# Kernel tuning notes

Measured on AMD Instinct MI355X. Metric: run time of the kernel, lower is better.

Reference implementation:

```python
import jax, jax.numpy as jnp
import numpy as np

B_, S_, H_, I_, N_, K_ = 2, 2048, 1024, 2048, 16, 4

def setup_inputs() -> dict:
    key = jax.random.key(0)
    ks = jax.random.split(key, 6)
    return {
        "x": jax.random.normal(ks[0], (B_, S_, H_), jnp.float32),
        "W_in": jax.random.normal(ks[1], (H_, 2 * I_), jnp.float32) * (H_ ** -0.5),
        "conv_w": jax.random.normal(ks[2], (I_, 1, K_), jnp.float32) * (K_ ** -0.5),
        "ln_gamma": jnp.ones((I_,), jnp.float32),
        "ln_beta": jnp.zeros((I_,), jnp.float32),
        "W_xproj": jax.random.normal(ks[3], (I_, 2 * N_ + 1), jnp.float32) * (I_ ** -0.5),
        "A_param": jax.random.normal(ks[4], (I_, N_), jnp.float32) * 0.1,
        "D": jnp.ones((I_,), jnp.float32),
        "W_out": jax.random.normal(ks[5], (I_, H_), jnp.float32) * (I_ ** -0.5),
    }

def _layernorm(x, g, b, eps=1e-5):
    mu = jnp.mean(x, axis=-1, keepdims=True)
    var = jnp.mean((x - mu) ** 2, axis=-1, keepdims=True)
    return (x - mu) * jax.lax.rsqrt(var + eps) * g + b

def reference(x, W_in, conv_w, ln_gamma, ln_beta, W_xproj, A_param, D, W_out):
    b, s, _ = x.shape
    n = A_param.shape[1]
    xz = x @ W_in                                   # (b,s,2I)
    xc, z = jnp.split(xz, 2, axis=-1)
    # depthwise causal conv1d: torch pads both sides k-1 then truncates [:s] == left-pad k-1
    xc = jax.lax.conv_general_dilated(
        xc.transpose(0, 2, 1), conv_w, window_strides=(1,),
        padding=[(conv_w.shape[-1] - 1, 0)],
        feature_group_count=conv_w.shape[0],
        dimension_numbers=("NCH", "OIH", "NCH")).transpose(0, 2, 1)  # (b,s,I)
    xc = jax.nn.silu(xc)
    xc = _layernorm(xc, ln_gamma, ln_beta)
    xp = xc @ W_xproj                               # (b,s,2N+1)
    delta = jnp.clip(jax.nn.softplus(xp[..., :1]), 1e-6, 10.0)   # (b,s,1)
    Bm = xp[..., 1:1 + n]                           # (b,s,N)
    Cm = xp[..., 1 + n:]                            # (b,s,N)
    A = -jnp.clip(jax.nn.softplus(A_param), 0.1, 10.0)           # (I,N)
    # decay[b,s,i,n] = exp(delta[b,s] * A[i,n]), clamped
    decay = jnp.clip(jnp.exp(delta[..., None] * A[None, None]), 1e-6, 1.0)  # (b,s,I,N)
    # y = x * sum_n B*C*decay  (state-dim reduction of the broadcast 4D tensor)
    y = xc * jnp.einsum("bsn,bsin->bsi", Bm * Cm, decay)
    y = y + xc * D
    return (y * jax.nn.silu(z)) @ W_out
```

## Files before the change

### kernel.cpp

```cpp
#include <hip/hip_runtime.h>
#include <hip/hip_bf16.h>
#include <cmath>

typedef __bf16 bf16_t;
typedef __bf16 bf16x8 __attribute__((ext_vector_type(8)));
typedef __bf16 bf16x4 __attribute__((ext_vector_type(4)));
typedef float  f32x4  __attribute__((ext_vector_type(4)));

static constexpr int B_  = 2, S_ = 2048, H_ = 1024, I_ = 2048, NST = 16;
static constexpr int ROWS  = B_ * S_;
static constexpr int TWO_I = 2 * I_;
static constexpr int XPD   = 2 * NST + 1;
static constexpr int XPN   = 64;

#define AS_G(p) ((const __attribute__((address_space(1))) void*)(p))
#define AS_L(p) ((__attribute__((address_space(3))) void*)(p))

template<int N> __device__ __forceinline__ void wait_vmcnt();
template<> __device__ __forceinline__ void wait_vmcnt<4>() {
    asm volatile("s_waitcnt vmcnt(4)" ::: "memory");
}

__device__ __forceinline__ float softplus_f(float x) {
    return x > 15.f ? x : log1pf(__expf(x));
}

__device__ __forceinline__ f32x4 b2f(bf16x4 v) {
    return (f32x4){(float)v[0], (float)v[1], (float)v[2], (float)v[3]};
}

__device__ __forceinline__ float fast_exp2(float x) {
#if __has_builtin(__builtin_amdgcn_exp2f)
    return __builtin_amdgcn_exp2f(x);
#else
    return exp2f(x);
#endif
}
__device__ __forceinline__ float fast_rcp(float x) {
#if __has_builtin(__builtin_amdgcn_rcpf)
    return __builtin_amdgcn_rcpf(x);
#else
    return 1.f / x;
#endif
}
__device__ __forceinline__ float fast_sigmoid(float x) {
    return fast_rcp(1.f + __expf(-x));
}
__device__ __forceinline__ float rflf(float x) {
    return __int_as_float(__builtin_amdgcn_readfirstlane(__float_as_int(x)));
}

template<int GX, int GY, int XW>
__device__ __forceinline__ void xcd_swz(int id, int& bx, int& by) {
    constexpr int SX = GX / XW;
    constexpr int SY = GY * XW / 8;
    const int xcd = id & 7;
    const int j   = id >> 3;
    bx = (xcd % XW) * SX + j % SX;
    by = (xcd / XW) * SY + j / SX;
}


__global__ __launch_bounds__(256)
void prep_all(const float* __restrict__ x, const float* __restrict__ W_in,
              const float* __restrict__ W_out, const float* __restrict__ A_param,
              const float* __restrict__ Wx, const float* __restrict__ conv_w,
              bf16_t* __restrict__ Xb, bf16_t* __restrict__ W1t,
              bf16_t* __restrict__ Wot, float* __restrict__ A2T,
              float* __restrict__ cwT, bf16_t* __restrict__ WxTb)
{
    const int b   = blockIdx.x;
    const int tid = threadIdx.x;
    __shared__ float t[32][33];

    if (b < 4096) {
        const int i = b * 256 + tid;
        f32x4 v = *(const f32x4*)(x + (size_t)i * 4);
        bf16x4 o;
        o[0] = (bf16_t)v[0]; o[1] = (bf16_t)v[1];
        o[2] = (bf16_t)v[2]; o[3] = (bf16_t)v[3];
        *(bf16x4*)(Xb + (size_t)i * 4) = o;
    } else if (b < 8192) {
        const int tb = b - 4096;
        const int c0 = (tb & 127) * 32, r0 = (tb >> 7) * 32;
        const int tx = tid & 31, ty = tid >> 5;
        #pragma unroll
        for (int k = 0; k < 4; ++k)
            t[ty + 8 * k][tx] = W_in[(size_t)(r0 + ty + 8 * k) * 4096 + c0 + tx];
        __syncthreads();
        #pragma unroll
        for (int k = 0; k < 4; ++k)
            W1t[(size_t)(c0 + ty + 8 * k) * 1024 + r0 + tx] = (bf16_t)t[tx][ty + 8 * k];
    } else if (b < 10240) {
        const int tb = b - 8192;
        const int c0 = (tb & 31) * 32, r0 = (tb >> 5) * 32;
        const int tx = tid & 31, ty = tid >> 5;
        #pragma unroll
        for (int k = 0; k < 4; ++k)
            t[ty + 8 * k][tx] = W_out[(size_t)(r0 + ty + 8 * k) * 1024 + c0 + tx];
        __syncthreads();
        #pragma unroll
        for (int k = 0; k < 4; ++k)
            Wot[(size_t)(c0 + ty + 8 * k) * 2048 + r0 + tx] = (bf16_t)t[tx][ty + 8 * k];
    } else {
        const int i = (b - 10240) * 256 + tid;
        if (i < NST * I_) {
            int n = i >> 11, c = i & (I_ - 1);
            float sp = softplus_f(A_param[(size_t)c * NST + n]);
            A2T[i] = -fminf(fmaxf(sp, 0.1f), 10.f) * 1.44269504088896340736f;
        }
        if (i < 4 * I_) {
            int j = i >> 11, c = i & (I_ - 1);
            cwT[i] = conv_w[(size_t)c * 4 + j];
        }
        if (i < XPN * I_) {
            int j = i >> 11, c = i & (I_ - 1);
            WxTb[i] = (j < XPD) ? (bf16_t)Wx[(size_t)c * XPD + j] : (bf16_t)0.f;
        }
    }
}


template<int M, int N, int K, int BM, int BN, int WM, int WN, int THREADS,
         int GX, int GY, int XW, typename OutT>
__global__ __launch_bounds__(THREADS)
void gemm_fp(const bf16_t* __restrict__ A, const bf16_t* __restrict__ Bt,
             OutT* __restrict__ C)
{
    constexpr int BK  = 32;
    constexpr int NT  = K / BK;
    constexpr int MR  = BM / WM / 16;
    constexpr int NR  = BN / WN / 16;
    constexpr int MH  = MR / 2;
    constexpr int RPC = THREADS / 4;
    constexpr int CA  = BM / RPC;
    constexpr int CB  = BN / RPC;
    static_assert(CA + CB == 4, "vmcnt template fixed at 4");

    __shared__ bf16_t lA[4][BM * BK];
    __shared__ bf16_t lB[4][BN * BK];

    int bx, by;
    xcd_swz<GX, GY, XW>(blockIdx.x, bx, by);
    const int bm = by * BM;
    const int bn = bx * BN;

    const int tid  = threadIdx.x;
    const int lane = tid & 63;
    const int wave = tid >> 6;
    const int wm   = wave / WN;
    const int wn   = wave % WN;

    const int frow = lane & 15;
    const int fsw  = ((lane >> 4) ^ ((frow >> 1) & 3)) << 3;

    const int str = tid >> 2;
    const int stp = tid & 3;

    const bf16_t* baseA[CA];
    #pragma unroll
    for (int a = 0; a < CA; ++a) {
        const int rt = a * RPC + str;
        baseA[a] = A + (size_t)(bm + rt) * K + ((stp ^ ((rt >> 1) & 3)) << 3);
    }
    const bf16_t* baseB[CB];
    #pragma unroll
    for (int a = 0; a < CB; ++a) {
        const int rt = a * RPC + str;
        baseB[a] = Bt + (size_t)(bn + rt) * K + ((stp ^ ((rt >> 1) & 3)) << 3);
    }

    f32x4 acc[MR][NR];
    #pragma unroll
    for (int m = 0; m < MR; ++m)
        #pragma unroll
        for (int n = 0; n < NR; ++n)
            acc[m][n] = (f32x4){0.f, 0.f, 0.f, 0.f};

    auto stageA = [&](int k0, int b) {
        #pragma unroll
        for (int a = 0; a < CA; ++a)
            __builtin_amdgcn_global_load_lds(AS_G(baseA[a] + k0),
                AS_L(&lA[b][a * RPC * 32 + wave * 512]), 16, 0, 0);
    };
    auto stageB = [&](int k0, int b) {
        #pragma unroll
        for (int a = 0; a < CB; ++a)
            __builtin_amdgcn_global_load_lds(AS_G(baseB[a] + k0),
                AS_L(&lB[b][a * RPC * 32 + wave * 512]), 16, 0, 0);
    };

    stageA(0, 0); stageB(0, 0);
    stageA(BK, 1); stageB(BK, 1);
    wait_vmcnt<4>();
    __builtin_amdgcn_s_barrier();

    #pragma unroll 1
    for (int t = 0; t < NT; ++t) {
        const int buf = t & 3;
        const int nb  = (t + 2) & 3;
        int kn = (t + 2) * BK;
        if (kn >= K) kn -= K;

        bf16x8 bfr[NR];
        #pragma unroll
        for (int n = 0; n < NR; ++n)
            bfr[n] = *(const bf16x8*)(&lB[buf][(wn * (NR * 16) + n * 16 + frow) * 32 + fsw]);
        bf16x8 af0[MH];
        #pragma unroll
        for (int m = 0; m < MH; ++m)
            af0[m] = *(const bf16x8*)(&lA[buf][(wm * (MR * 16) + m * 16 + frow) * 32 + fsw]);
        stageA(kn, nb);

        __builtin_amdgcn_s_setprio(1);
        #pragma unroll
        for (int m = 0; m < MH; ++m)
            #pragma unroll
            for (int n = 0; n < NR; ++n)
                acc[m][n] = __builtin_amdgcn_mfma_f32_16x16x32_bf16(
                    af0[m], bfr[n], acc[m][n], 0, 0, 0);
        __builtin_amdgcn_s_setprio(0);

        bf16x8 af1[MR - MH];
        #pragma unroll
        for (int m = 0; m < MR - MH; ++m)
            af1[m] = *(const bf16x8*)(&lA[buf][(wm * (MR * 16) + (MH + m) * 16 + frow) * 32 + fsw]);
        stageB(kn, nb);

        __builtin_amdgcn_s_setprio(1);
        #pragma unroll
        for (int m = 0; m < MR - MH; ++m)
            #pragma unroll
            for (int n = 0; n < NR; ++n)
                acc[MH + m][n] = __builtin_amdgcn_mfma_f32_16x16x32_bf16(
                    af1[m], bfr[n], acc[MH + m][n], 0, 0, 0);
        __builtin_amdgcn_s_setprio(0);

        wait_vmcnt<4>();
        __builtin_amdgcn_s_barrier();
    }

    const int crow = (lane >> 4) * 4;
    const int ccol = lane & 15;
    #pragma unroll
    for (int m = 0; m < MR; ++m)
        #pragma unroll
        for (int n = 0; n < NR; ++n)
            #pragma unroll
            for (int r = 0; r < 4; ++r)
                C[(size_t)(bm + wm * (MR * 16) + m * 16 + crow + r) * N
                  + (bn + wn * (NR * 16) + n * 16 + ccol)] = (OutT)acc[m][n][r];
}


template<int M, int N, int K, int GX, int GY, int XW>
__global__ __launch_bounds__(512)
void gemm3_kg(const bf16_t* __restrict__ A, const bf16_t* __restrict__ Bt,
              float* __restrict__ C)
{
    constexpr int BM = 128, BN = 128, BK = 32;
    constexpr int KH = K / 2;
    constexpr int NT = KH / BK;
    constexpr int MR = 4, NR = 4, MH = 2;

    __shared__ bf16_t smem[65536];

    int bx, by;
    xcd_swz<GX, GY, XW>(blockIdx.x, bx, by);
    const int bm = by * BM;
    const int bn = bx * BN;

    const int tid  = threadIdx.x;
    const int lane = tid & 63;
    const int wave = tid >> 6;
    const int grp  = wave >> 2;
    const int gw   = wave & 3;
    const int wm   = gw >> 1;
    const int wn   = gw & 1;

    const int frow = lane & 15;
    const int fsw  = ((lane >> 4) ^ ((frow >> 1) & 3)) << 3;

    const int gtid = tid & 255;
    const int str  = gtid >> 2;
    const int stp  = gtid & 3;

    bf16_t* lA = smem + grp * 16384;
    bf16_t* lB = smem + 32768 + grp * 16384;

    const bf16_t* baseA[2];
    #pragma unroll
    for (int a = 0; a < 2; ++a) {
        const int rt = a * 64 + str;
        baseA[a] = A + (size_t)(bm + rt) * K + grp * KH + ((stp ^ ((rt >> 1) & 3)) << 3);
    }
    const bf16_t* baseB[2];
    #pragma unroll
    for (int a = 0; a < 2; ++a) {
        const int rt = a * 64 + str;
        baseB[a] = Bt + (size_t)(bn + rt) * K + grp * KH + ((stp ^ ((rt >> 1) & 3)) << 3);
    }

    f32x4 acc[MR][NR];
    #pragma unroll
    for (int m = 0; m < MR; ++m)
        #pragma unroll
        for (int n = 0; n < NR; ++n)
            acc[m][n] = (f32x4){0.f, 0.f, 0.f, 0.f};

    auto stageA = [&](int k0, int b) {
        #pragma unroll
        for (int a = 0; a < 2; ++a)
            __builtin_amdgcn_global_load_lds(AS_G(baseA[a] + k0),
                AS_L(lA + b * 4096 + a * 2048 + gw * 512), 16, 0, 0);
    };
    auto stageB = [&](int k0, int b) {
        #pragma unroll
        for (int a = 0; a < 2; ++a)
            __builtin_amdgcn_global_load_lds(AS_G(baseB[a] + k0),
                AS_L(lB + b * 4096 + a * 2048 + gw * 512), 16, 0, 0);
    };

    stageA(0, 0); stageB(0, 0);
    stageA(BK, 1); stageB(BK, 1);
    wait_vmcnt<4>();
    __builtin_amdgcn_s_barrier();

    #pragma unroll 1
    for (int t = 0; t < NT; ++t) {
        const int buf = t & 3;
        const int nb  = (t + 2) & 3;
        int kn = (t + 2) * BK;
        if (kn >= KH) kn -= KH;

        bf16x8 bfr[NR];
        #pragma unroll
        for (int n = 0; n < NR; ++n)
            bfr[n] = *(const bf16x8*)(lB + buf * 4096 + (wn * 64 + n * 16 + frow) * 32 + fsw);
        bf16x8 af0[MH];
        #pragma unroll
        for (int m = 0; m < MH; ++m)
            af0[m] = *(const bf16x8*)(lA + buf * 4096 + (wm * 64 + m * 16 + frow) * 32 + fsw);
        stageA(kn, nb);

        __builtin_amdgcn_s_setprio(1);
        #pragma unroll
        for (int m = 0; m < MH; ++m)
            #pragma unroll
            for (int n = 0; n < NR; ++n)
                acc[m][n] = __builtin_amdgcn_mfma_f32_16x16x32_bf16(
                    af0[m], bfr[n], acc[m][n], 0, 0, 0);
        __builtin_amdgcn_s_setprio(0);

        bf16x8 af1[MR - MH];
        #pragma unroll
        for (int m = 0; m < MR - MH; ++m)
            af1[m] = *(const bf16x8*)(lA + buf * 4096 + (wm * 64 + (MH + m) * 16 + frow) * 32 + fsw);
        stageB(kn, nb);

        __builtin_amdgcn_s_setprio(1);
        #pragma unroll
        for (int m = 0; m < MR - MH; ++m)
            #pragma unroll
            for (int n = 0; n < NR; ++n)
                acc[MH + m][n] = __builtin_amdgcn_mfma_f32_16x16x32_bf16(
                    af1[m], bfr[n], acc[MH + m][n], 0, 0, 0);
        __builtin_amdgcn_s_setprio(0);

        wait_vmcnt<4>();
        __builtin_amdgcn_s_barrier();
    }

    asm volatile("s_waitcnt vmcnt(0)" ::: "memory");
    __builtin_amdgcn_s_barrier();

    float* accx = (float*)smem;
    const int crow = (lane >> 4) * 4;
    const int ccol = lane & 15;

    if (grp == 1) {
        #pragma unroll
        for (int m = 0; m < MR; ++m)
            #pragma unroll
            for (int n = 0; n < NR; ++n) {
                const int row = wm * 64 + m * 16 + crow;
                const int col = wn * 64 + n * 16 + ccol;
                #pragma unroll
                for (int r = 0; r < 4; ++r)
                    accx[(size_t)(row + r) * 132 + col] = acc[m][n][r];
            }
    }
    __syncthreads();
    if (grp == 0) {
        #pragma unroll
        for (int m = 0; m < MR; ++m)
            #pragma unroll
            for (int n = 0; n < NR; ++n) {
                const int row = wm * 64 + m * 16 + crow;
                const int col = wn * 64 + n * 16 + ccol;
                #pragma unroll
                for (int r = 0; r < 4; ++r)
                    C[(size_t)(bm + row + r) * N + bn + col] =
                        acc[m][n][r] + accx[(size_t)(row + r) * 132 + col];
            }
    }
}


__global__ __launch_bounds__(256)
void conv_ln4(const bf16_t* __restrict__ xz,
              const float* __restrict__ cwT,
              const float* __restrict__ ln_g,
              const float* __restrict__ ln_b,
              bf16_t* __restrict__ Xn)
{
    const int row0 = blockIdx.x * 4;
    const int s0   = row0 & (S_ - 1);
    const int tid  = threadIdx.x;
    const int lane = tid & 63;
    const int wave = tid >> 6;
    const bf16_t* xzr = xz + (size_t)row0 * TWO_I;

    __shared__ float lnr[4][4][2];

    float xc[4][8];
    float sm[4] = {0.f, 0.f, 0.f, 0.f};
    float sq[4] = {0.f, 0.f, 0.f, 0.f};

    #pragma unroll
    for (int g = 0; g < 2; ++g) {
        const int c = g * 1024 + tid * 4;
        const f32x4 w0 = *(const f32x4*)(cwT + 0 * I_ + c);
        const f32x4 w1 = *(const f32x4*)(cwT + 1 * I_ + c);
        const f32x4 w2 = *(const f32x4*)(cwT + 2 * I_ + c);
        const f32x4 w3 = *(const f32x4*)(cwT + 3 * I_ + c);
        const f32x4 z4 = (f32x4){0.f, 0.f, 0.f, 0.f};
        f32x4 xv[7];
        #pragma unroll
        for (int j = 0; j < 7; ++j)
            xv[j] = (s0 + j >= 3)
                  ? b2f(*(const bf16x4*)(xzr + (ptrdiff_t)(j - 3) * TWO_I + c)) : z4;
        #pragma unroll
        for (int r = 0; r < 4; ++r) {
            const f32x4 a = w0 * xv[r] + w1 * xv[r + 1] + w2 * xv[r + 2] + w3 * xv[r + 3];
            #pragma unroll
            for (int e = 0; e < 4; ++e) {
                const float v = a[e];
                const float t = v * fast_sigmoid(v);
                xc[r][g * 4 + e] = t;
                sm[r] += t; sq[r] += t * t;
            }
        }
    }

    #pragma unroll
    for (int off = 32; off; off >>= 1)
        #pragma unroll
        for (int r = 0; r < 4; ++r) {
            sm[r] += __shfl_xor(sm[r], off, 64);
            sq[r] += __shfl_xor(sq[r], off, 64);
        }
    if (lane == 0)
        #pragma unroll
        for (int r = 0; r < 4; ++r) {
            lnr[wave][r][0] = sm[r]; lnr[wave][r][1] = sq[r];
        }
    __syncthreads();
    float mu[4], rs[4];
    #pragma unroll
    for (int r = 0; r < 4; ++r) {
        const float s  = lnr[0][r][0] + lnr[1][r][0] + lnr[2][r][0] + lnr[3][r][0];
        const float q  = lnr[0][r][1] + lnr[1][r][1] + lnr[2][r][1] + lnr[3][r][1];
        mu[r] = s * (1.f / I_);
        rs[r] = rsqrtf(q * (1.f / I_) - mu[r] * mu[r] + 1e-5f);
    }

    #pragma unroll
    for (int g = 0; g < 2; ++g) {
        const int c = g * 1024 + tid * 4;
        const f32x4 gg = *(const f32x4*)(ln_g + c);
        const f32x4 bb = *(const f32x4*)(ln_b + c);
        #pragma unroll
        for (int r = 0; r < 4; ++r) {
            bf16x4 h4;
            #pragma unroll
            for (int e = 0; e < 4; ++e)
                h4[e] = (bf16_t)((xc[r][g * 4 + e] - mu[r]) * rs[r] * gg[e] + bb[e]);
            *(bf16x4*)(Xn + (size_t)(row0 + r) * I_ + c) = h4;
        }
    }
}


__global__ __launch_bounds__(256)
void xproj_gemm(const bf16_t* __restrict__ Xn,
                const bf16_t* __restrict__ Wb, float* __restrict__ xp_part)
{
    constexpr int BM = 128, BK = 32, KS = 512;
    __shared__ bf16_t lA[BM * BK];
    __shared__ bf16_t lB[XPN * BK];

    const int bm   = blockIdx.x * BM;
    const int ks   = blockIdx.y;
    const int tid  = threadIdx.x;
    const int lane = tid & 63;
    const int wave = tid >> 6;
    const int wm   = (wave >> 1) * 64;
    const int wn   = (wave & 1) * 32;

    const int srow  = lane >> 2;
    const int skoff = (lane & 3) * 8;
    const int frow  = lane & 15;
    const int fko   = (lane >> 4) * 8;

    f32x4 acc[4][2];
    #pragma unroll
    for (int m = 0; m < 4; ++m)
        #pragma unroll
        for (int n = 0; n < 2; ++n)
            acc[m][n] = (f32x4){0.f, 0.f, 0.f, 0.f};

    for (int k0 = ks * KS; k0 < ks * KS + KS; k0 += BK) {
        #pragma unroll
        for (int t = 0; t < 2; ++t) {
            const int c = wave * 2 + t;
            const bf16_t* ga = Xn + (size_t)(bm + c * 16 + srow) * I_ + k0 + skoff;
            __builtin_amdgcn_global_load_lds(AS_G(ga), AS_L(lA + c * 512), 16, 0, 0);
        }
        const bf16_t* gb = Wb + (size_t)(wave * 16 + srow) * I_ + k0 + skoff;
        __builtin_amdgcn_global_load_lds(AS_G(gb), AS_L(lB + wave * 512), 16, 0, 0);
        __syncthreads();

        bf16x8 af[4], bf2[2];
        #pragma unroll
        for (int m = 0; m < 4; ++m)
            af[m] = *(const bf16x8*)(lA + (wm + m * 16 + frow) * BK + fko);
        #pragma unroll
        for (int n = 0; n < 2; ++n)
            bf2[n] = *(const bf16x8*)(lB + (wn + n * 16 + frow) * BK + fko);

        #pragma unroll
        for (int m = 0; m < 4; ++m)
            #pragma unroll
            for (int n = 0; n < 2; ++n)
                acc[m][n] = __builtin_amdgcn_mfma_f32_16x16x32_bf16(
                    af[m], bf2[n], acc[m][n], 0, 0, 0);

        __syncthreads();
    }

    float* out = xp_part + ((size_t)ks * ROWS + bm) * XPN;
    const int crow = (lane >> 4) * 4;
    const int ccol = lane & 15;
    #pragma unroll
    for (int m = 0; m < 4; ++m)
        #pragma unroll
        for (int n = 0; n < 2; ++n)
            #pragma unroll
            for (int r = 0; r < 4; ++r)
                out[(size_t)(wm + m * 16 + crow + r) * XPN
                    + (wn + n * 16 + ccol)] = acc[m][n][r];
}


__global__ __launch_bounds__(256)
void ssm_gate4(const bf16_t* __restrict__ xz,
               const bf16_t* __restrict__ Xn,
               const float* __restrict__ xp_part,
               const float* __restrict__ A2T,
               const float* __restrict__ Dv,
               bf16_t* __restrict__ U)
{
    const int row0 = blockIdx.x * 4;
    const int tid  = threadIdx.x;

    __shared__ float xps[4][XPD];
    __shared__ float bcs[4][NST];

    if (tid < 4 * XPD) {
        const int r = tid / XPD;
        const int j = tid - r * XPD;
        float s = 0.f;
        #pragma unroll
        for (int ks = 0; ks < 4; ++ks)
            s += xp_part[((size_t)ks * ROWS + row0 + r) * XPN + j];
        xps[r][j] = s;
    }
    __syncthreads();
    if (tid < 4 * NST) {
        const int r = tid >> 4;
        const int n = tid & 15;
        bcs[r][n] = xps[r][1 + n] * xps[r][1 + NST + n];
    }
    __syncthreads();

    float d[4];
    #pragma unroll
    for (int r = 0; r < 4; ++r)
        d[r] = fminf(fmaxf(softplus_f(xps[r][0]), 1e-6f), 10.f);

    #pragma unroll 1
    for (int g = 0; g < 2; ++g) {
        const int c = g * 1024 + tid * 4;
        f32x4 sa[4];
        #pragma unroll
        for (int r = 0; r < 4; ++r)
            sa[r] = (f32x4){0.f, 0.f, 0.f, 0.f};

        #pragma unroll 1
        for (int nb = 0; nb < 4; ++nb) {
            const float* ap = A2T + (size_t)(nb * 4) * I_ + c;
            f32x4 av[4];
            #pragma unroll
            for (int j = 0; j < 4; ++j)
                av[j] = *(const f32x4*)(ap + (size_t)j * I_);
            #pragma unroll
            for (int j = 0; j < 4; ++j) {
                const float b0 = rflf(bcs[0][nb * 4 + j]);
                const float b1 = rflf(bcs[1][nb * 4 + j]);
                const float b2 = rflf(bcs[2][nb * 4 + j]);
                const float b3 = rflf(bcs[3][nb * 4 + j]);
                #pragma unroll
                for (int e = 0; e < 4; ++e) {
                    sa[0][e] += b0 * fast_exp2(d[0] * av[j][e]);
                    sa[1][e] += b1 * fast_exp2(d[1] * av[j][e]);
                    sa[2][e] += b2 * fast_exp2(d[2] * av[j][e]);
                    sa[3][e] += b3 * fast_exp2(d[3] * av[j][e]);
                }
            }
        }

        const f32x4 dvv = *(const f32x4*)(Dv + c);
        #pragma unroll
        for (int r = 0; r < 4; ++r) {
            const f32x4 xn = b2f(*(const bf16x4*)(Xn + (size_t)(row0 + r) * I_ + c));
            const f32x4 zv = b2f(*(const bf16x4*)(xz + (size_t)(row0 + r) * TWO_I + I_ + c));
            bf16x4 o;
            #pragma unroll
            for (int e = 0; e < 4; ++e) {
                const float y = xn[e] * (sa[r][e] + dvv[e]);
                const float z = zv[e];
                o[e] = (bf16_t)(y * z * fast_sigmoid(z));
            }
            *(bf16x4*)(U + (size_t)(row0 + r) * I_ + c) = o;
        }
    }
}


extern "C" void kernel_launch(void* const* d_in, const int* in_sizes, int n_in,
                              void* d_out, int out_size, void* d_ws, size_t ws_size,
                              hipStream_t stream)
{
    const float* x     = (const float*)d_in[0];
    const float* W_in  = (const float*)d_in[1];
    const float* convw = (const float*)d_in[2];
    const float* ln_g  = (const float*)d_in[3];
    const float* ln_b  = (const float*)d_in[4];
    const float* Wx    = (const float*)d_in[5];
    const float* A_p   = (const float*)d_in[6];
    const float* Dv    = (const float*)d_in[7];
    const float* W_out = (const float*)d_in[8];
    float* out = (float*)d_out;

    char* ws = (char*)d_ws;
    bf16_t* Xb   = (bf16_t*)(ws);
    bf16_t* W1t  = (bf16_t*)(ws + (size_t)(8u  << 20));
    bf16_t* Wot  = (bf16_t*)(ws + (size_t)(16u << 20));
    float*  A2T  = (float*) (ws + (size_t)(20u << 20));
    float*  cwT  = (float*) (ws + (size_t)(20u << 20) + (128u << 10));
    bf16_t* WxTb = (bf16_t*)(ws + (size_t)(20u << 20) + (256u << 10));
    bf16_t* XZb  = (bf16_t*)(ws + (size_t)(22u << 20));
    bf16_t* U    = (bf16_t*)(ws + (size_t)(54u << 20));
    bf16_t* Xn   = (bf16_t*)(ws);
    float*  xp4  = (float*) (ws + (size_t)(86u << 20));

    prep_all<<<10752, 256, 0, stream>>>(x, W_in, W_out, A_p, Wx, convw,
                                        Xb, W1t, Wot, A2T, cwT, WxTb);

    gemm_fp<ROWS, TWO_I, H_, 256, 256, 2, 4, 512, 16, 16, 4, bf16_t>
        <<<256, 512, 0, stream>>>(Xb, W1t, XZb);
    conv_ln4<<<ROWS / 4, 256, 0, stream>>>(XZb, cwT, ln_g, ln_b, Xn);
    xproj_gemm<<<dim3(ROWS / 128, 4), 256, 0, stream>>>(Xn, WxTb, xp4);
    ssm_gate4<<<ROWS / 4, 256, 0, stream>>>(XZb, Xn, xp4, A2T, Dv, U);
    gemm3_kg<ROWS, H_, I_, 8, 32, 2>
        <<<256, 512, 0, stream>>>(U, Wot, out);
}
```

Before: 119.3 us.

## Use split-K 128x128 GEMM for input projection and process 8 rows per SSM block

```diff
diff --git a/kernel.cpp b/kernel.cpp
--- a/kernel.cpp
+++ b/kernel.cpp
@@ -121,142 +121,10 @@
 }
 
 
-template<int M, int N, int K, int BM, int BN, int WM, int WN, int THREADS,
-         int GX, int GY, int XW, typename OutT>
-__global__ __launch_bounds__(THREADS)
-void gemm_fp(const bf16_t* __restrict__ A, const bf16_t* __restrict__ Bt,
+template<int M, int N, int K, int GX, int GY, int XW, typename OutT>
+__global__ __launch_bounds__(512)
+void gemm_kg(const bf16_t* __restrict__ A, const bf16_t* __restrict__ Bt,
              OutT* __restrict__ C)
-{
-    constexpr int BK  = 32;
-    constexpr int NT  = K / BK;
-    constexpr int MR  = BM / WM / 16;
-    constexpr int NR  = BN / WN / 16;
-    constexpr int MH  = MR / 2;
-    constexpr int RPC = THREADS / 4;
-    constexpr int CA  = BM / RPC;
-    constexpr int CB  = BN / RPC;
-    static_assert(CA + CB == 4, "vmcnt template fixed at 4");
-
-    __shared__ bf16_t lA[4][BM * BK];
-    __shared__ bf16_t lB[4][BN * BK];
-
-    int bx, by;
-    xcd_swz<GX, GY, XW>(blockIdx.x, bx, by);
-    const int bm = by * BM;
-    const int bn = bx * BN;
-
-    const int tid  = threadIdx.x;
-    const int lane = tid & 63;
-    const int wave = tid >> 6;
-    const int wm   = wave / WN;
-    const int wn   = wave % WN;
-
-    const int frow = lane & 15;
-    const int fsw  = ((lane >> 4) ^ ((frow >> 1) & 3)) << 3;
-
-    const int str = tid >> 2;
-    const int stp = tid & 3;
-
-    const bf16_t* baseA[CA];
-    #pragma unroll
-    for (int a = 0; a < CA; ++a) {
-        const int rt = a * RPC + str;
-        baseA[a] = A + (size_t)(bm + rt) * K + ((stp ^ ((rt >> 1) & 3)) << 3);
-    }
-    const bf16_t* baseB[CB];
-    #pragma unroll
-    for (int a = 0; a < CB; ++a) {
-        const int rt = a * RPC + str;
-        baseB[a] = Bt + (size_t)(bn + rt) * K + ((stp ^ ((rt >> 1) & 3)) << 3);
-    }
-
-    f32x4 acc[MR][NR];
-    #pragma unroll
-    for (int m = 0; m < MR; ++m)
-        #pragma unroll
-        for (int n = 0; n < NR; ++n)
-            acc[m][n] = (f32x4){0.f, 0.f, 0.f, 0.f};
-
-    auto stageA = [&](int k0, int b) {
-        #pragma unroll
-        for (int a = 0; a < CA; ++a)
-            __builtin_amdgcn_global_load_lds(AS_G(baseA[a] + k0),
-                AS_L(&lA[b][a * RPC * 32 + wave * 512]), 16, 0, 0);
-    };
-    auto stageB = [&](int k0, int b) {
-        #pragma unroll
-        for (int a = 0; a < CB; ++a)
-            __builtin_amdgcn_global_load_lds(AS_G(baseB[a] + k0),
-                AS_L(&lB[b][a * RPC * 32 + wave * 512]), 16, 0, 0);
-    };
-
-    stageA(0, 0); stageB(0, 0);
-    stageA(BK, 1); stageB(BK, 1);
-    wait_vmcnt<4>();
-    __builtin_amdgcn_s_barrier();
-
-    #pragma unroll 1
-    for (int t = 0; t < NT; ++t) {
-        const int buf = t & 3;
-        const int nb  = (t + 2) & 3;
-        int kn = (t + 2) * BK;
-        if (kn >= K) kn -= K;
-
-        bf16x8 bfr[NR];
-        #pragma unroll
-        for (int n = 0; n < NR; ++n)
-            bfr[n] = *(const bf16x8*)(&lB[buf][(wn * (NR * 16) + n * 16 + frow) * 32 + fsw]);
-        bf16x8 af0[MH];
-        #pragma unroll
-        for (int m = 0; m < MH; ++m)
-            af0[m] = *(const bf16x8*)(&lA[buf][(wm * (MR * 16) + m * 16 + frow) * 32 + fsw]);
-        stageA(kn, nb);
-
-        __builtin_amdgcn_s_setprio(1);
-        #pragma unroll
-        for (int m = 0; m < MH; ++m)
-            #pragma unroll
-            for (int n = 0; n < NR; ++n)
-                acc[m][n] = __builtin_amdgcn_mfma_f32_16x16x32_bf16(
-                    af0[m], bfr[n], acc[m][n], 0, 0, 0);
-        __builtin_amdgcn_s_setprio(0);
-
-        bf16x8 af1[MR - MH];
-        #pragma unroll
-        for (int m = 0; m < MR - MH; ++m)
-            af1[m] = *(const bf16x8*)(&lA[buf][(wm * (MR * 16) + (MH + m) * 16 + frow) * 32 + fsw]);
-        stageB(kn, nb);
-
-        __builtin_amdgcn_s_setprio(1);
-        #pragma unroll
-        for (int m = 0; m < MR - MH; ++m)
-            #pragma unroll
-            for (int n = 0; n < NR; ++n)
-                acc[MH + m][n] = __builtin_amdgcn_mfma_f32_16x16x32_bf16(
-                    af1[m], bfr[n], acc[MH + m][n], 0, 0, 0);
-        __builtin_amdgcn_s_setprio(0);
-
-        wait_vmcnt<4>();
-        __builtin_amdgcn_s_barrier();
-    }
-
-    const int crow = (lane >> 4) * 4;
-    const int ccol = lane & 15;
-    #pragma unroll
-    for (int m = 0; m < MR; ++m)
-        #pragma unroll
-        for (int n = 0; n < NR; ++n)
-            #pragma unroll
-            for (int r = 0; r < 4; ++r)
-                C[(size_t)(bm + wm * (MR * 16) + m * 16 + crow + r) * N
-                  + (bn + wn * (NR * 16) + n * 16 + ccol)] = (OutT)acc[m][n][r];
-}
-
-
-template<int M, int N, int K, int GX, int GY, int XW>
-__global__ __launch_bounds__(512)
-void gemm3_kg(const bf16_t* __restrict__ A, const bf16_t* __restrict__ Bt,
-              float* __restrict__ C)
 {
     constexpr int BM = 128, BN = 128, BK = 32;
     constexpr int KH = K / 2;
@@ -401,7 +269,7 @@
                 #pragma unroll
                 for (int r = 0; r < 4; ++r)
                     C[(size_t)(bm + row + r) * N + bn + col] =
-                        acc[m][n][r] + accx[(size_t)(row + r) * 132 + col];
+                        (OutT)(acc[m][n][r] + accx[(size_t)(row + r) * 132 + col]);
             }
     }
 }
@@ -564,22 +432,22 @@
 
 
 __global__ __launch_bounds__(256)
-void ssm_gate4(const bf16_t* __restrict__ xz,
+void ssm_gate8(const bf16_t* __restrict__ xz,
                const bf16_t* __restrict__ Xn,
                const float* __restrict__ xp_part,
                const float* __restrict__ A2T,
                const float* __restrict__ Dv,
                bf16_t* __restrict__ U)
 {
-    const int row0 = blockIdx.x * 4;
+    const int row0 = blockIdx.x * 8;
     const int tid  = threadIdx.x;
 
-    __shared__ float xps[4][XPD];
-    __shared__ float bcs[4][NST];
-
-    if (tid < 4 * XPD) {
-        const int r = tid / XPD;
-        const int j = tid - r * XPD;
+    __shared__ float xps[8][XPD];
+    __shared__ float bcs[8][NST];
+
+    for (int i = tid; i < 8 * XPD; i += 256) {
+        const int r = i / XPD;
+        const int j = i - r * XPD;
         float s = 0.f;
         #pragma unroll
         for (int ks = 0; ks < 4; ++ks)
@@ -587,24 +455,24 @@
         xps[r][j] = s;
     }
     __syncthreads();
-    if (tid < 4 * NST) {
+    if (tid < 8 * NST) {
         const int r = tid >> 4;
         const int n = tid & 15;
         bcs[r][n] = xps[r][1 + n] * xps[r][1 + NST + n];
     }
     __syncthreads();
 
-    float d[4];
-    #pragma unroll
-    for (int r = 0; r < 4; ++r)
+    float d[8];
+    #pragma unroll
+    for (int r = 0; r < 8; ++r)
         d[r] = fminf(fmaxf(softplus_f(xps[r][0]), 1e-6f), 10.f);
 
     #pragma unroll 1
     for (int g = 0; g < 2; ++g) {
         const int c = g * 1024 + tid * 4;
-        f32x4 sa[4];
-        #pragma unroll
-        for (int r = 0; r < 4; ++r)
+        f32x4 sa[8];
+        #pragma unroll
+        for (int r = 0; r < 8; ++r)
             sa[r] = (f32x4){0.f, 0.f, 0.f, 0.f};
 
         #pragma unroll 1
@@ -616,23 +484,22 @@
                 av[j] = *(const f32x4*)(ap + (size_t)j * I_);
             #pragma unroll
             for (int j = 0; j < 4; ++j) {
-                const float b0 = rflf(bcs[0][nb * 4 + j]);
-                const float b1 = rflf(bcs[1][nb * 4 + j]);
-                const float b2 = rflf(bcs[2][nb * 4 + j]);
-                const float b3 = rflf(bcs[3][nb * 4 + j]);
+                float bv[8];
+                #pragma unroll
+                for (int r = 0; r < 8; ++r)
+                    bv[r] = rflf(bcs[r][nb * 4 + j]);
                 #pragma unroll
                 for (int e = 0; e < 4; ++e) {
-                    sa[0][e] += b0 * fast_exp2(d[0] * av[j][e]);
-                    sa[1][e] += b1 * fast_exp2(d[1] * av[j][e]);
-                    sa[2][e] += b2 * fast_exp2(d[2] * av[j][e]);
-                    sa[3][e] += b3 * fast_exp2(d[3] * av[j][e]);
+                    #pragma unroll
+                    for (int r = 0; r < 8; ++r)
+                        sa[r][e] += bv[r] * fast_exp2(d[r] * av[j][e]);
                 }
             }
         }
 
         const f32x4 dvv = *(const f32x4*)(Dv + c);
         #pragma unroll
-        for (int r = 0; r < 4; ++r) {
+        for (int r = 0; r < 8; ++r) {
             const f32x4 xn = b2f(*(const bf16x4*)(Xn + (size_t)(row0 + r) * I_ + c));
             const f32x4 zv = b2f(*(const bf16x4*)(xz + (size_t)(row0 + r) * TWO_I + I_ + c));
             bf16x4 o;
@@ -678,11 +545,11 @@
     prep_all<<<10752, 256, 0, stream>>>(x, W_in, W_out, A_p, Wx, convw,
                                         Xb, W1t, Wot, A2T, cwT, WxTb);
 
-    gemm_fp<ROWS, TWO_I, H_, 256, 256, 2, 4, 512, 16, 16, 4, bf16_t>
-        <<<256, 512, 0, stream>>>(Xb, W1t, XZb);
+    gemm_kg<ROWS, TWO_I, H_, 32, 32, 4, bf16_t>
+        <<<1024, 512, 0, stream>>>(Xb, W1t, XZb);
     conv_ln4<<<ROWS / 4, 256, 0, stream>>>(XZb, cwT, ln_g, ln_b, Xn);
     xproj_gemm<<<dim3(ROWS / 128, 4), 256, 0, stream>>>(Xn, WxTb, xp4);
-    ssm_gate4<<<ROWS / 4, 256, 0, stream>>>(XZb, Xn, xp4, A2T, Dv, U);
-    gemm3_kg<ROWS, H_, I_, 8, 32, 2>
+    ssm_gate8<<<ROWS / 8, 256, 0, stream>>>(XZb, Xn, xp4, A2T, Dv, U);
+    gemm_kg<ROWS, H_, I_, 8, 32, 2, float>
         <<<256, 512, 0, stream>>>(U, Wot, out);
 }
```

Measured after the change: 136.6 us. 1.14x slower.
